# Kernel optimization log

Measured on AMD Instinct MI355X. Metric: run time of the kernel, lower is better.

## Reference

```python
import jax, jax.numpy as jnp
import numpy as np

N, EG, T, H, EC, L, NT = 10000, 200000, 300000, 128, 128, 3, 100


def _ssp(x):
    # ShiftedSoftplus: softplus(x) - log(2)
    return jax.nn.softplus(x) - jnp.log(2.0).astype(x.dtype)


def _bn(x, g, b):
    # BatchNorm1d in training mode: biased batch stats, eps=1e-5
    m = jnp.mean(x, axis=0)
    v = jnp.var(x, axis=0)
    return g * (x - m) * jax.lax.rsqrt(v + 1e-5) + b


def _forward(z, i, j, idx_i, idx_j, idx_k, idx_ji, idx_kj, pos,
             We1, be1, We2, be2, We3, be3,
             Wc1, bc1, g_c1, b_c1, g_n, b_n,
             Wc2, bc2, g_c2, b_c2, Wc3, bc3, g_c3, b_c3,
             g_c22, b_c22, g_c32, b_c32,
             Wf1, bf1, Wf2, bf2, Wf3, bf3):
    # AtomType2NodeEmb
    h = jax.nn.one_hot(z, NT, dtype=jnp.float32)
    h = _ssp(h @ We1 + be1)
    h = _ssp(h @ We2 + be2)
    node = h @ We3 + be3                      # [N, H]
    # geometry + GaussianFilter edge embedding
    rel = pos[i] - pos[j]                     # [EG, 3]
    dist = jnp.sqrt(jnp.sum(rel * rel, axis=-1))
    unit = rel / dist[:, None]
    offset = jnp.linspace(0.0, 5.0, EC)
    coeff = -0.5 / (offset[1] - offset[0]) ** 2
    edge = jnp.exp(coeff * (dist[:, None] - offset[None, :]) ** 2)  # [EG, EC]
    for l in range(L):
        # NodeUpdate
        c1 = jnp.concatenate([node[i], edge], axis=1) @ Wc1[l] + bc1[l]
        c1 = _bn(c1, g_c1[l], b_c1[l])
        f1, r1 = jnp.split(c1, 2, axis=1)
        agg = jax.ops.segment_sum(jax.nn.sigmoid(f1) * jnp.tanh(r1), i, num_segments=N)
        node = jnp.tanh(node + _bn(agg, g_n[l], b_n[l]))
        # EdgeUpdate: pair term
        c2 = (node[i] * node[j]) @ Wc2[l] + bc2[l]
        c2 = _bn(c2, g_c2[l], b_c2[l])
        f2, r2 = jnp.split(c2, 2, axis=1)
        c2_emb = _bn(jax.nn.sigmoid(f2) * jnp.tanh(r2), g_c22[l], b_c22[l])
        # EdgeUpdate: triplet term
        c3 = jnp.concatenate([node[idx_i], node[idx_j], node[idx_k],
                              edge[idx_ji], edge[idx_kj]], axis=1) @ Wc3[l] + bc3[l]
        c3 = _bn(c3, g_c3[l], b_c3[l])
        f3, r3 = jnp.split(c3, 2, axis=1)
        agg3 = jax.ops.segment_sum(jax.nn.sigmoid(f3) * jnp.tanh(r3), idx_ji, num_segments=EG)
        c3_emb = _bn(agg3, g_c32[l], b_c32[l])
        edge = jnp.tanh(edge + c2_emb + c3_emb)
    # ForcePredictor
    f = _ssp(edge @ Wf1 + bf1)
    f = _ssp(f @ Wf2 + bf2)
    force = (f @ Wf3 + bf3) * unit            # [EG, 3]
    return jax.ops.segment_sum(force, i, num_segments=N)


def setup_inputs() -> dict:
    ks = iter(jax.random.split(jax.random.key(0), 32))

    def w(shape):
        return jax.random.normal(next(ks), shape, jnp.float32) * (shape[-2] ** -0.5)

    z = jax.random.randint(next(ks), (N,), 0, NT)
    pos = jax.random.uniform(next(ks), (N, 3), jnp.float32) * 5.0
    i = jax.random.randint(next(ks), (EG,), 0, N)
    j = (i + 1 + jax.random.randint(next(ks), (EG,), 0, N - 1)) % N  # no self-loops
    idx_i = jax.random.randint(next(ks), (T,), 0, N)
    idx_j = jax.random.randint(next(ks), (T,), 0, N)
    idx_k = jax.random.randint(next(ks), (T,), 0, N)
    idx_ji = jax.random.randint(next(ks), (T,), 0, EG)
    idx_kj = jax.random.randint(next(ks), (T,), 0, EG)
    return dict(
        z=z, pos=pos, i=i, j=j, idx_i=idx_i, idx_j=idx_j, idx_k=idx_k,
        idx_ji=idx_ji, idx_kj=idx_kj,
        We1=w((NT, H)), be1=jnp.zeros((H,)), We2=w((H, H)), be2=jnp.zeros((H,)),
        We3=w((H, H)), be3=jnp.zeros((H,)),
        Wc1=w((L, H + EC, 2 * H)), bc1=jnp.zeros((L, 2 * H)),
        g_c1=jnp.ones((L, 2 * H)), b_c1=jnp.zeros((L, 2 * H)),
        g_n=jnp.ones((L, H)), b_n=jnp.zeros((L, H)),
        Wc2=w((L, H, 2 * EC)), bc2=jnp.zeros((L, 2 * EC)),
        g_c2=jnp.ones((L, 2 * EC)), b_c2=jnp.zeros((L, 2 * EC)),
        Wc3=w((L, 3 * H + 2 * EC, 2 * EC)), bc3=jnp.zeros((L, 2 * EC)),
        g_c3=jnp.ones((L, 2 * EC)), b_c3=jnp.zeros((L, 2 * EC)),
        g_c22=jnp.ones((L, EC)), b_c22=jnp.zeros((L, EC)),
        g_c32=jnp.ones((L, EC)), b_c32=jnp.zeros((L, EC)),
        Wf1=w((EC, EC)), bf1=jnp.zeros((EC,)), Wf2=w((EC, EC)), bf2=jnp.zeros((EC,)),
        Wf3=w((EC, 1)), bf3=jnp.zeros((1,)),
    )


def reference(z, pos, i, j, idx_i, idx_j, idx_k, idx_ji, idx_kj,
              We1, be1, We2, be2, We3, be3,
              Wc1, bc1, g_c1, b_c1, g_n, b_n,
              Wc2, bc2, g_c2, b_c2, Wc3, bc3, g_c3, b_c3,
              g_c22, b_c22, g_c32, b_c32,
              Wf1, bf1, Wf2, bf2, Wf3, bf3):
    return _forward(z, i, j, idx_i, idx_j, idx_k, idx_ji, idx_kj, pos,
                    We1, be1, We2, be2, We3, be3,
                    Wc1, bc1, g_c1, b_c1, g_n, b_n,
                    Wc2, bc2, g_c2, b_c2, Wc3, bc3, g_c3, b_c3,
                    g_c22, b_c22, g_c32, b_c32,
                    Wf1, bf1, Wf2, bf2, Wf3, bf3)
```

## Files before the change

kernel.cpp:

```cpp
#include <hip/hip_runtime.h>

typedef unsigned short u16;
typedef unsigned int   u32;
typedef __attribute__((ext_vector_type(8))) short short8;
typedef __attribute__((ext_vector_type(4))) float f32x4;

#define NN  10000
#define EGN 200000
#define TTN 300000
#define LLN 3

__device__ __forceinline__ float b2f(u16 u){ union{u32 i; float f;} x; x.i=(u32)u<<16; return x.f; }
__device__ __forceinline__ u16 f2b(float f){ union{float f; u32 u;} x; x.f=f; u32 r=(x.u + 0x7fffu + ((x.u>>16)&1u))>>16; return (u16)r; }
__device__ __forceinline__ float sigf(float x){ return 1.f/(1.f+__expf(-x)); }
__device__ __forceinline__ float tanhf_(float x){ float e=__expf(2.f*x); return 1.f - 2.f/(e+1.f); }
__device__ __forceinline__ float sspf(float x){ return fmaxf(x,0.f) + log1pf(__expf(-fabsf(x))) - 0.6931471805599453f; }

__device__ __forceinline__ void async16(void* lds, const void* g){
  __builtin_amdgcn_global_load_lds((const __attribute__((address_space(1))) void*)g,
                                   (__attribute__((address_space(3))) void*)lds, 16, 0, 0);
}
__device__ __forceinline__ void split_store(float v, u16* ph, u16* pl, size_t o){
  u16 h = f2b(v); ph[o] = h; pl[o] = f2b(v - b2f(h));
}
__device__ __forceinline__ short8 ldfrag(const u16* P, int row, int kk, int lane){
  int kg = kk*4 + (lane>>4);
  int slot = kg ^ (row&7);
  return *(const short8*)(P + row*64 + slot*8);
}

struct Segs {
  const u16* sh[10];
  const u16* sl[10];
  const int* idx[10];
  int coff[10];
};

template<int NP, int ROWS>
__device__ __forceinline__ void stageA(u16* Ah, u16* Al,
    const u16* sh, const u16* sl, const int* idxp, int coff,
    int rb, int M, int tid){
#pragma unroll
  for (int rnd=0; rnd<ROWS/32; ++rnd){
    int u = rnd*256 + tid;
    int row = u>>3, s = u&7, sw = s ^ (row&7);
    int grow = rb + row; if (grow >= M) grow = M-1;
    int srow = idxp ? idxp[grow] : grow;
    size_t go = (size_t)srow*256 + coff + sw*16;
    async16(Ah + u*8, (const char*)sh + go);
    if (NP==2) async16(Al + u*8, (const char*)sl + go);
  }
}

template<int NP, int ROWS>
__device__ __forceinline__ void stageA_prod(u16* Ah, u16* Al,
    const u16* nh, const u16* nl, const int* pii, const int* pjj,
    int rb, int M, int ks, int tid){
#pragma unroll
  for (int rep=0; rep<ROWS/64; ++rep){
    int row = rep*64 + (tid>>2), q = tid&3;
    int e = rb + row; if (e >= M) e = M-1;
    int ia = pii[e], ja = pjj[e];
    const u16* phi = nh + (size_t)ia*128 + ks*64 + q*16;
    const u16* pli = nl + (size_t)ia*128 + ks*64 + q*16;
    const u16* phj = nh + (size_t)ja*128 + ks*64 + q*16;
    const u16* plj = nl + (size_t)ja*128 + ks*64 + q*16;
#pragma unroll
    for (int c=0;c<2;c++){
      short8 hi = *(const short8*)(phi + c*8);
      short8 li = *(const short8*)(pli + c*8);
      short8 hj = *(const short8*)(phj + c*8);
      short8 lj = *(const short8*)(plj + c*8);
      short8 vh, vl;
#pragma unroll
      for (int k=0;k<8;k++){
        float a = b2f((u16)hi[k]) + b2f((u16)li[k]);
        float b = b2f((u16)hj[k]) + b2f((u16)lj[k]);
        float v = a*b;
        u16 h = f2b(v);
        vh[k] = (short)h;
        vl[k] = (short)f2b(v - b2f(h));
      }
      int g = q*2 + c, slot = g ^ (row&7);
      *(short8*)(Ah + row*64 + slot*8) = vh;
      if (NP==2) *(short8*)(Al + row*64 + slot*8) = vl;
    }
  }
}

template<int NP, int BROWS>
__device__ __forceinline__ void stageB_id(u16* Bh, u16* Bl,
    const u16* Wh, const u16* Wl, int K2b, int ksoff, int tid){
#pragma unroll
  for (int rnd=0; rnd<BROWS/32; ++rnd){
    int u = rnd*256 + tid;
    int row = u>>3, s = u&7, sw = s ^ (row&7);
    size_t go = (size_t)row*K2b + ksoff + sw*16;
    async16(Bh + u*8, (const char*)Wh + go);
    if (NP==2) async16(Bl + u*8, (const char*)Wl + go);
  }
}

template<int NP>
__device__ __forceinline__ void stageB_pair(u16* Bh, u16* Bl,
    const u16* Wh, const u16* Wl, int P0, int K2b, int ksoff, int tid){
#pragma unroll
  for (int rnd=0; rnd<4; ++rnd){
    int u = rnd*256 + tid;
    int row = u>>3, s = u&7, sw = s ^ (row&7);
    int wr = (row < 64) ? (P0 + row) : (128 + P0 + (row-64));
    size_t go = (size_t)wr*K2b + ksoff + sw*16;
    async16(Bh + u*8, (const char*)Wh + go);
    if (NP==2) async16(Bl + u*8, (const char*)Wl + go);
  }
}

template<bool PROD>
__global__ __launch_bounds__(256) void gemm_stats(
  int M, int nseg, Segs segs,
  const u16* __restrict__ nh, const u16* __restrict__ nl,
  const int* __restrict__ pii, const int* __restrict__ pjj,
  const u16* __restrict__ Wh, int K2b, const float* __restrict__ bias,
  float* __restrict__ st)
{
  __shared__ u16 Ah[64*64];
  __shared__ u16 Bh[256*64];
  __shared__ float ls[256], lq[256];
  const int tid = threadIdx.x, lane = tid&63, wv = tid>>6;
  const int rb = blockIdx.x*64;
  ls[tid]=0.f; lq[tid]=0.f;

  f32x4 acc[16];
#pragma unroll
  for (int n=0;n<16;n++) acc[n] = (f32x4){0.f,0.f,0.f,0.f};

  for (int ks=0; ks<nseg; ++ks){
    if (PROD) stageA_prod<1,64>(Ah, nullptr, nh, nl, pii, pjj, rb, M, ks, tid);
    else      stageA<1,64>(Ah, nullptr, segs.sh[ks], nullptr, segs.idx[ks], segs.coff[ks], rb, M, tid);
    stageB_id<1,256>(Bh, nullptr, Wh, nullptr, K2b, ks*128, tid);
    __syncthreads();
    const int arow = wv*16 + (lane&15);
#pragma unroll
    for (int kk=0;kk<2;kk++){
      short8 a = ldfrag(Ah, arow, kk, lane);
#pragma unroll
      for (int n=0;n<16;n++){
        short8 b = ldfrag(Bh, n*16 + (lane&15), kk, lane);
        acc[n] = __builtin_amdgcn_mfma_f32_16x16x32_bf16(a, b, acc[n], 0,0,0);
      }
    }
    __syncthreads();
  }
#pragma unroll
  for (int n=0;n<16;n++){
    float bb = bias[n*16 + (lane&15)];
    float s=0.f, q=0.f;
#pragma unroll
    for (int r=0;r<4;r++){
      int grow = rb + wv*16 + (lane>>4)*4 + r;
      if (grow < M){ float v = acc[n][r] + bb; s += v; q += v*v; }
    }
    s += __shfl_xor(s,16); s += __shfl_xor(s,32);
    q += __shfl_xor(q,16); q += __shfl_xor(q,32);
    if (lane < 16){ atomicAdd(&ls[n*16+lane], s); atomicAdd(&lq[n*16+lane], q); }
  }
  __syncthreads();
  atomicAdd(&st[tid], ls[tid]); atomicAdd(&st[256+tid], lq[tid]);
}

template<int NP, bool PROD, int EPI>
__global__ __launch_bounds__(256) void gemm_pair(
  int M, int nseg, Segs segs,
  const u16* __restrict__ nh, const u16* __restrict__ nl,
  const int* __restrict__ pii, const int* __restrict__ pjj,
  const u16* __restrict__ Wh, const u16* __restrict__ Wl, int K2b,
  const float* __restrict__ bias,
  const float* __restrict__ st, const float* __restrict__ g, const float* __restrict__ b, float inv,
  const int* __restrict__ sidx, float* __restrict__ aggout,
  const float* __restrict__ st22, const float* __restrict__ g22, const float* __restrict__ b22,
  const float* __restrict__ st32, const float* __restrict__ g32, const float* __restrict__ b32, float inv2,
  const float* __restrict__ agg3, u16* __restrict__ eh, u16* __restrict__ el,
  float* __restrict__ st22out)
{
  __shared__ u16 Ah[128*64];
  __shared__ u16 Al[NP==2 ? 128*64 : 64];
  __shared__ u16 Bh[128*64];
  __shared__ u16 Bl[NP==2 ? 128*64 : 64];
  __shared__ float ls[64], lq[64];
  __shared__ float sAf[64], sCf[64], sAr[64], sCr[64];
  __shared__ float sA22[64], sC22[64], sA32[64], sC32[64];
  const int tid = threadIdx.x, lane = tid&63, wv = tid>>6;
  const int wm = wv>>1, wn = wv&1;
  const int rb = blockIdx.x*128, P0 = blockIdx.y*64;

  if (tid < 64){
    int p = P0 + tid;
    float m1 = st[p]*inv,     v1 = st[256+p]*inv - m1*m1;
    float a1 = g[p]*rsqrtf(v1+1e-5f);
    sAf[tid]=a1; sCf[tid]=b[p]-a1*m1;
    float m2 = st[128+p]*inv, v2 = st[384+p]*inv - m2*m2;
    float a2 = g[128+p]*rsqrtf(v2+1e-5f);
    sAr[tid]=a2; sCr[tid]=b[128+p]-a2*m2;
    if (EPI==1){
      float m3 = st22[p]*inv2, v3 = st22[128+p]*inv2 - m3*m3;
      float a3 = g22[p]*rsqrtf(v3+1e-5f);
      sA22[tid]=a3; sC22[tid]=b22[p]-a3*m3;
      float m4 = st32[p]*inv2, v4 = st32[128+p]*inv2 - m4*m4;
      float a4 = g32[p]*rsqrtf(v4+1e-5f);
      sA32[tid]=a4; sC32[tid]=b32[p]-a4*m4;
    }
    if (EPI==2){ ls[tid]=0.f; lq[tid]=0.f; }
  }

  f32x4 accf[4][2], accr[4][2];
#pragma unroll
  for (int m=0;m<4;m++)
#pragma unroll
    for (int n=0;n<2;n++){ accf[m][n]=(f32x4){0.f,0.f,0.f,0.f}; accr[m][n]=(f32x4){0.f,0.f,0.f,0.f}; }

  for (int ks=0; ks<nseg; ++ks){
    if (PROD) stageA_prod<NP,128>(Ah, Al, nh, nl, pii, pjj, rb, M, ks, tid);
    else      stageA<NP,128>(Ah, Al, segs.sh[ks], segs.sl[ks], segs.idx[ks], segs.coff[ks], rb, M, tid);
    stageB_pair<NP>(Bh, Bl, Wh, Wl, P0, K2b, ks*128, tid);
    __syncthreads();
#pragma unroll
    for (int kk=0;kk<2;kk++){
      short8 ah[4], al[4];
#pragma unroll
      for (int m=0;m<4;m++){
        int ar = wm*64 + m*16 + (lane&15);
        ah[m] = ldfrag(Ah, ar, kk, lane);
        if constexpr (NP==2) al[m] = ldfrag(Al, ar, kk, lane);
      }
#pragma unroll
      for (int n=0;n<2;n++){
        int brf = wn*32 + n*16 + (lane&15);
        short8 bfh = ldfrag(Bh, brf,    kk, lane);
        short8 brh = ldfrag(Bh, 64+brf, kk, lane);
        short8 bfl, brl;
        if constexpr (NP==2){ bfl = ldfrag(Bl, brf, kk, lane); brl = ldfrag(Bl, 64+brf, kk, lane); }
#pragma unroll
        for (int m=0;m<4;m++){
          accf[m][n] = __builtin_amdgcn_mfma_f32_16x16x32_bf16(ah[m], bfh, accf[m][n], 0,0,0);
          accr[m][n] = __builtin_amdgcn_mfma_f32_16x16x32_bf16(ah[m], brh, accr[m][n], 0,0,0);
          if constexpr (NP==2){
            accf[m][n] = __builtin_amdgcn_mfma_f32_16x16x32_bf16(ah[m], bfl, accf[m][n], 0,0,0);
            accf[m][n] = __builtin_amdgcn_mfma_f32_16x16x32_bf16(al[m], bfh, accf[m][n], 0,0,0);
            accr[m][n] = __builtin_amdgcn_mfma_f32_16x16x32_bf16(ah[m], brl, accr[m][n], 0,0,0);
            accr[m][n] = __builtin_amdgcn_mfma_f32_16x16x32_bf16(al[m], brh, accr[m][n], 0,0,0);
          }
        }
      }
    }
    __syncthreads();
  }

#pragma unroll
  for (int n=0;n<2;n++){
    const int pp = wn*32 + n*16 + (lane&15);
    const int p  = P0 + pp;
    const float bf_ = bias[p], br_ = bias[128+p];
    const float Af = sAf[pp], Cf = sCf[pp], Ar = sAr[pp], Cr = sCr[pp];
    float su=0.f, sq=0.f;
#pragma unroll
    for (int m=0;m<4;m++){
#pragma unroll
      for (int r=0;r<4;r++){
        int grow = rb + wm*64 + m*16 + (lane>>4)*4 + r;
        if (grow < M){
          float yf = accf[m][n][r] + bf_;
          float yr = accr[m][n][r] + br_;
          float u = sigf(Af*yf + Cf) * tanhf_(Ar*yr + Cr);
          if (EPI==0){
            atomicAdd(&aggout[(size_t)sidx[grow]*128 + p], u);
          } else if (EPI==1){
            size_t o = (size_t)grow*128 + p;
            float eo = b2f(eh[o]) + b2f(el[o]);
            float v = tanhf_(eo + sA22[pp]*u + sC22[pp] + sA32[pp]*agg3[o] + sC32[pp]);
            split_store(v, eh, el, o);
          } else {
            su += u; sq += u*u;
          }
        }
      }
    }
    if (EPI==2){
      su += __shfl_xor(su,16); su += __shfl_xor(su,32);
      sq += __shfl_xor(sq,16); sq += __shfl_xor(sq,32);
      if (lane < 16){ atomicAdd(&ls[wn*32+n*16+lane], su); atomicAdd(&lq[wn*32+n*16+lane], sq); }
    }
  }
  if (EPI==2){
    __syncthreads();
    if (tid < 64){ atomicAdd(&st22out[P0+tid], ls[tid]); atomicAdd(&st22out[128+P0+tid], lq[tid]); }
  }
}

__global__ __launch_bounds__(256) void gemm_force(
  int M, Segs segs,
  const u16* __restrict__ Wh, const u16* __restrict__ Wl, int K2b,
  const float* __restrict__ bias, u16* __restrict__ oh, u16* __restrict__ ol)
{
  __shared__ u16 Ah[64*64], Al[64*64];
  __shared__ u16 Bh[128*64], Bl[128*64];
  const int tid = threadIdx.x, lane = tid&63, wv = tid>>6;
  const int rb = blockIdx.x*64;

  f32x4 acc[8];
#pragma unroll
  for (int n=0;n<8;n++) acc[n] = (f32x4){0.f,0.f,0.f,0.f};

  for (int ks=0; ks<2; ++ks){
    stageA<2,64>(Ah, Al, segs.sh[ks], segs.sl[ks], segs.idx[ks], segs.coff[ks], rb, M, tid);
    stageB_id<2,128>(Bh, Bl, Wh, Wl, K2b, ks*128, tid);
    __syncthreads();
    const int arow = wv*16 + (lane&15);
#pragma unroll
    for (int kk=0;kk<2;kk++){
      short8 ah = ldfrag(Ah, arow, kk, lane);
      short8 al = ldfrag(Al, arow, kk, lane);
#pragma unroll
      for (int n=0;n<8;n++){
        int br = n*16 + (lane&15);
        short8 bh = ldfrag(Bh, br, kk, lane);
        short8 bl = ldfrag(Bl, br, kk, lane);
        acc[n] = __builtin_amdgcn_mfma_f32_16x16x32_bf16(ah, bh, acc[n], 0,0,0);
        acc[n] = __builtin_amdgcn_mfma_f32_16x16x32_bf16(ah, bl, acc[n], 0,0,0);
        acc[n] = __builtin_amdgcn_mfma_f32_16x16x32_bf16(al, bh, acc[n], 0,0,0);
      }
    }
    __syncthreads();
  }
#pragma unroll
  for (int n=0;n<8;n++){
    int col = n*16 + (lane&15);
    float bb = bias[col];
#pragma unroll
    for (int r=0;r<4;r++){
      int grow = rb + wv*16 + (lane>>4)*4 + r;
      if (grow < M){
        float v = sspf(acc[n][r] + bb);
        split_store(v, oh, ol, (size_t)grow*128 + col);
      }
    }
  }
}

__global__ void transpose_cvt(const float* __restrict__ src, u16* __restrict__ dh, u16* __restrict__ dl, int K, int N){
  __shared__ float t[32][33];
  const float* s = src + (size_t)blockIdx.z * K * N;
  u16* dsth = dh + (size_t)blockIdx.z * K * N;
  u16* dstl = dl + (size_t)blockIdx.z * K * N;
  int n0 = blockIdx.x*32, k0 = blockIdx.y*32;
  for (int dy=threadIdx.y; dy<32; dy+=8){
    int k = k0+dy, n = n0+threadIdx.x;
    if (k<K && n<N) t[dy][threadIdx.x] = s[(size_t)k*N + n];
  }
  __syncthreads();
  for (int dy=threadIdx.y; dy<32; dy+=8){
    int n = n0+dy, k = k0+threadIdx.x;
    if (n<N && k<K) split_store(t[threadIdx.x][dy], dsth, dstl, (size_t)n*K + k);
  }
}

__global__ __launch_bounds__(128) void embed_k(const int* __restrict__ z,
  const float* __restrict__ We1, const float* __restrict__ be1,
  const float* __restrict__ We2, const float* __restrict__ be2,
  const float* __restrict__ We3, const float* __restrict__ be3,
  u16* __restrict__ nh, u16* __restrict__ nl){
  __shared__ float h0[128], h1[128];
  int nid = blockIdx.x, t = threadIdx.x;
  int zz = z[nid];
  h0[t] = sspf(We1[zz*128 + t] + be1[t]);
  __syncthreads();
  float a = be2[t];
  for (int k=0;k<128;k++) a += h0[k]*We2[k*128+t];
  h1[t] = sspf(a);
  __syncthreads();
  float b = be3[t];
  for (int k=0;k<128;k++) b += h1[k]*We3[k*128+t];
  split_store(b, nh, nl, (size_t)nid*128+t);
}

__global__ __launch_bounds__(256) void geom_k(const float* __restrict__ pos,
  const int* __restrict__ ii, const int* __restrict__ jj,
  float* __restrict__ unitv, u16* __restrict__ eh, u16* __restrict__ el){
  int t = threadIdx.x; int e = blockIdx.x*2 + (t>>7); int col = t&127;
  int a = ii[e], b = jj[e];
  float dx = pos[a*3]-pos[b*3], dy=pos[a*3+1]-pos[b*3+1], dz=pos[a*3+2]-pos[b*3+2];
  float dist = sqrtf(dx*dx+dy*dy+dz*dz);
  if (col==0){ float inv=1.f/dist; unitv[e*3]=dx*inv; unitv[e*3+1]=dy*inv; unitv[e*3+2]=dz*inv; }
  const float step = 5.0f/127.0f;
  const float coeff = -0.5f/(step*step);
  float d = dist - step*(float)col;
  float g = __expf(coeff*d*d);
  split_store(g, eh, el, (size_t)e*128+col);
}

__global__ __launch_bounds__(256) void colstats128(const float* __restrict__ m, int M, float* __restrict__ st){
  __shared__ float ls[128], lq[128];
  int t=threadIdx.x; if(t<128){ls[t]=0.f;lq[t]=0.f;} __syncthreads();
  int col=t&127, hf=t>>7; float ps=0.f,pq=0.f;
  int npair=(M+1)>>1;
  for (int pr=blockIdx.x; pr<npair; pr+=gridDim.x){
    int row=pr*2+hf;
    if(row<M){ float v=m[(size_t)row*128+col]; ps+=v; pq+=v*v; }
  }
  atomicAdd(&ls[col],ps); atomicAdd(&lq[col],pq);
  __syncthreads();
  if(t<128){ atomicAdd(&st[t],ls[t]); atomicAdd(&st[128+t],lq[t]); }
}

__global__ __launch_bounds__(256) void node_update_k(u16* __restrict__ nh, u16* __restrict__ nl,
  const float* __restrict__ agg, const float* __restrict__ st,
  const float* __restrict__ g, const float* __restrict__ b, float inv, int Nn)
{
  int t=threadIdx.x; int col=t&127, hf=t>>7;
  float mean = st[col]*inv;
  float var  = st[128+col]*inv - mean*mean;
  float A = g[col]*rsqrtf(var+1e-5f);
  float C = b[col] - A*mean;
  int npair=(Nn+1)>>1;
  for (int pr=blockIdx.x; pr<npair; pr+=gridDim.x){
    int row=pr*2+hf; if(row>=Nn) continue;
    size_t o=(size_t)row*128+col;
    float nv = b2f(nh[o]) + b2f(nl[o]);
    float v = tanhf_(nv + A*agg[o] + C);
    split_store(v, nh, nl, o);
  }
}

__global__ __launch_bounds__(256) void force_k(const u16* __restrict__ fh, const u16* __restrict__ fl,
  const float* __restrict__ Wf3, const float* __restrict__ bf3,
  const float* __restrict__ unitv, const int* __restrict__ ii, float* __restrict__ outp, int Me)
{
  int wv=threadIdx.x>>6, lane=threadIdx.x&63;
  int e = blockIdx.x*4 + wv; if(e>=Me) return;
  size_t o0=(size_t)e*128+lane, o1=o0+64;
  float p = (b2f(fh[o0])+b2f(fl[o0]))*Wf3[lane] + (b2f(fh[o1])+b2f(fl[o1]))*Wf3[64+lane];
  for (int s=32;s>0;s>>=1) p += __shfl_down(p, s);
  if (lane==0){
    float F = p + bf3[0];
    atomicAdd(&outp[ii[e]*3+0], F*unitv[e*3+0]);
    atomicAdd(&outp[ii[e]*3+1], F*unitv[e*3+1]);
    atomicAdd(&outp[ii[e]*3+2], F*unitv[e*3+2]);
  }
}

__global__ void sentinel_k(float* o, int n, float v){
  int i = blockIdx.x*256 + threadIdx.x; if (i<n) o[i]=v;
}

extern "C" void kernel_launch(void* const* d_in, const int* in_sizes, int n_in,
                              void* d_out, int out_size, void* d_ws, size_t ws_size,
                              hipStream_t stream)
{
  (void)in_sizes; (void)n_in;
  const int* z      = (const int*)d_in[0];
  const float* pos  = (const float*)d_in[1];
  const int* ii     = (const int*)d_in[2];
  const int* jj     = (const int*)d_in[3];
  const int* idx_i  = (const int*)d_in[4];
  const int* idx_j  = (const int*)d_in[5];
  const int* idx_k  = (const int*)d_in[6];
  const int* idx_ji = (const int*)d_in[7];
  const int* idx_kj = (const int*)d_in[8];
  const float* We1=(const float*)d_in[9];  const float* be1=(const float*)d_in[10];
  const float* We2=(const float*)d_in[11]; const float* be2=(const float*)d_in[12];
  const float* We3=(const float*)d_in[13]; const float* be3=(const float*)d_in[14];
  const float* Wc1=(const float*)d_in[15]; const float* bc1=(const float*)d_in[16];
  const float* g_c1=(const float*)d_in[17]; const float* b_c1=(const float*)d_in[18];
  const float* g_n=(const float*)d_in[19]; const float* b_n=(const float*)d_in[20];
  const float* Wc2=(const float*)d_in[21]; const float* bc2=(const float*)d_in[22];
  const float* g_c2=(const float*)d_in[23]; const float* b_c2=(const float*)d_in[24];
  const float* Wc3=(const float*)d_in[25]; const float* bc3=(const float*)d_in[26];
  const float* g_c3=(const float*)d_in[27]; const float* b_c3=(const float*)d_in[28];
  const float* g_c22=(const float*)d_in[29]; const float* b_c22=(const float*)d_in[30];
  const float* g_c32=(const float*)d_in[31]; const float* b_c32=(const float*)d_in[32];
  const float* Wf1=(const float*)d_in[33]; const float* bf1=(const float*)d_in[34];
  const float* Wf2=(const float*)d_in[35]; const float* bf2=(const float*)d_in[36];
  const float* Wf3=(const float*)d_in[37]; const float* bf3=(const float*)d_in[38];

  char* ws = (char*)d_ws;
  size_t off=0;
  auto alloc=[&](size_t b){ size_t o=off; off += (b+255)&~(size_t)255; return o; };
  u16*   node_h = (u16*)(ws + alloc((size_t)NN*128*2));
  u16*   node_l = (u16*)(ws + alloc((size_t)NN*128*2));
  u16*   edge_h = (u16*)(ws + alloc((size_t)EGN*128*2));
  u16*   edge_l = (u16*)(ws + alloc((size_t)EGN*128*2));
  float* unitv  = (float*)(ws + alloc((size_t)EGN*3*4));
  float* agg    = (float*)(ws + alloc((size_t)NN*128*4));
  float* agg3   = (float*)(ws + alloc((size_t)EGN*128*4));
  u16*   wc1h   = (u16*)(ws + alloc((size_t)3*256*256*2));
  u16*   wc1l   = (u16*)(ws + alloc((size_t)3*256*256*2));
  u16*   wc2h   = (u16*)(ws + alloc((size_t)3*256*128*2));
  u16*   wc2l   = (u16*)(ws + alloc((size_t)3*256*128*2));
  u16*   wc3h   = (u16*)(ws + alloc((size_t)3*256*640*2));
  u16*   wc3l   = (u16*)(ws + alloc((size_t)3*256*640*2));
  u16*   wf1h   = (u16*)(ws + alloc((size_t)128*128*2));
  u16*   wf1l   = (u16*)(ws + alloc((size_t)128*128*2));
  u16*   wf2h   = (u16*)(ws + alloc((size_t)128*128*2));
  u16*   wf2l   = (u16*)(ws + alloc((size_t)128*128*2));
  float* stats  = (float*)(ws + alloc(2304*4));

  if (off > ws_size){
    sentinel_k<<<(out_size+255)/256, 256, 0, stream>>>((float*)d_out, out_size, 123456.0f);
    return;
  }

  float* st1 = stats;
  float* st2 = stats+512;
  float* st3 = stats+1024;
  float* stN = stats+1536;
  float* st32= stats+1792;
  float* st22= stats+2048;

  u16* f1h = (u16*)agg3;
  u16* f1l = f1h + (size_t)EGN*128;
  u16* f2h = edge_h;
  u16* f2l = edge_l;

  hipMemsetAsync(d_out, 0, (size_t)out_size*4, stream);

  dim3 tb(32,8);
  transpose_cvt<<<dim3(8,8,3),  tb, 0, stream>>>(Wc1, wc1h, wc1l, 256, 256);
  transpose_cvt<<<dim3(8,4,3),  tb, 0, stream>>>(Wc2, wc2h, wc2l, 128, 256);
  transpose_cvt<<<dim3(8,20,3), tb, 0, stream>>>(Wc3, wc3h, wc3l, 640, 256);
  transpose_cvt<<<dim3(4,4,1),  tb, 0, stream>>>(Wf1, wf1h, wf1l, 128, 128);
  transpose_cvt<<<dim3(4,4,1),  tb, 0, stream>>>(Wf2, wf2h, wf2l, 128, 128);

  embed_k<<<NN,128,0,stream>>>(z, We1,be1,We2,be2,We3,be3, node_h, node_l);
  geom_k<<<EGN/2,256,0,stream>>>(pos, ii, jj, unitv, edge_h, edge_l);

  const int gE64  = (EGN+63)/64;
  const int gT64  = (TTN+63)/64;
  const int gE128 = (EGN+127)/128;
  const int gT128 = (TTN+127)/128;
  Segs dummy{};
  const float invE = 1.0f/EGN, invT = 1.0f/TTN, invN = 1.0f/NN;

  for (int l=0;l<LLN;l++){
    hipMemsetAsync(stats, 0, 2304*4, stream);
    hipMemsetAsync(agg,  0, (size_t)NN*128*4, stream);
    hipMemsetAsync(agg3, 0, (size_t)EGN*128*4, stream);

    const u16* w1h = wc1h + l*256*256; const u16* w1l = wc1l + l*256*256;
    const u16* w2h = wc2h + l*256*128; const u16* w2l = wc2l + l*256*128;
    const u16* w3h = wc3h + l*256*640; const u16* w3l = wc3l + l*256*640;

    Segs s1{};
    s1.sh[0]=node_h; s1.sl[0]=node_l; s1.idx[0]=ii;      s1.coff[0]=0;
    s1.sh[1]=node_h; s1.sl[1]=node_l; s1.idx[1]=ii;      s1.coff[1]=128;
    s1.sh[2]=edge_h; s1.sl[2]=edge_l; s1.idx[2]=nullptr; s1.coff[2]=0;
    s1.sh[3]=edge_h; s1.sl[3]=edge_l; s1.idx[3]=nullptr; s1.coff[3]=128;
    gemm_stats<false><<<gE64,256,0,stream>>>(EGN, 4, s1, nullptr,nullptr,nullptr,nullptr,
                                             w1h, 512, bc1+l*256, st1);
    gemm_pair<2,false,0><<<dim3(gE128,2),256,0,stream>>>(EGN, 4, s1, nullptr,nullptr,nullptr,nullptr,
        w1h, w1l, 512, bc1+l*256,
        st1, g_c1+l*256, b_c1+l*256, invE,
        ii, agg,
        nullptr,nullptr,nullptr, nullptr,nullptr,nullptr, 0.f,
        nullptr, nullptr, nullptr, nullptr);
    colstats128<<<256,256,0,stream>>>(agg, NN, stN);
    node_update_k<<<2048,256,0,stream>>>(node_h, node_l, agg, stN, g_n+l*128, b_n+l*128, invN, NN);

    Segs s3{};
    s3.sh[0]=node_h; s3.sl[0]=node_l; s3.idx[0]=idx_i;  s3.coff[0]=0;
    s3.sh[1]=node_h; s3.sl[1]=node_l; s3.idx[1]=idx_i;  s3.coff[1]=128;
    s3.sh[2]=node_h; s3.sl[2]=node_l; s3.idx[2]=idx_j;  s3.coff[2]=0;
    s3.sh[3]=node_h; s3.sl[3]=node_l; s3.idx[3]=idx_j;  s3.coff[3]=128;
    s3.sh[4]=node_h; s3.sl[4]=node_l; s3.idx[4]=idx_k;  s3.coff[4]=0;
    s3.sh[5]=node_h; s3.sl[5]=node_l; s3.idx[5]=idx_k;  s3.coff[5]=128;
    s3.sh[6]=edge_h; s3.sl[6]=edge_l; s3.idx[6]=idx_ji; s3.coff[6]=0;
    s3.sh[7]=edge_h; s3.sl[7]=edge_l; s3.idx[7]=idx_ji; s3.coff[7]=128;
    s3.sh[8]=edge_h; s3.sl[8]=edge_l; s3.idx[8]=idx_kj; s3.coff[8]=0;
    s3.sh[9]=edge_h; s3.sl[9]=edge_l; s3.idx[9]=idx_kj; s3.coff[9]=128;
    gemm_stats<false><<<gT64,256,0,stream>>>(TTN, 10, s3, nullptr,nullptr,nullptr,nullptr,
                                             w3h, 1280, bc3+l*256, st3);
    gemm_pair<2,false,0><<<dim3(gT128,2),256,0,stream>>>(TTN, 10, s3, nullptr,nullptr,nullptr,nullptr,
        w3h, w3l, 1280, bc3+l*256,
        st3, g_c3+l*256, b_c3+l*256, invT,
        idx_ji, agg3,
        nullptr,nullptr,nullptr, nullptr,nullptr,nullptr, 0.f,
        nullptr, nullptr, nullptr, nullptr);
    colstats128<<<1024,256,0,stream>>>(agg3, EGN, st32);

    gemm_stats<true><<<gE64,256,0,stream>>>(EGN, 2, dummy, node_h,node_l,ii,jj,
                                            w2h, 256, bc2+l*256, st2);
    gemm_pair<1,true,2><<<dim3(gE128,2),256,0,stream>>>(EGN, 2, dummy, node_h,node_l,ii,jj,
        w2h, nullptr, 256, bc2+l*256,
        st2, g_c2+l*256, b_c2+l*256, invE,
        nullptr, nullptr,
        nullptr,nullptr,nullptr, nullptr,nullptr,nullptr, 0.f,
        nullptr, nullptr, nullptr, st22);
    gemm_pair<2,true,1><<<dim3(gE128,2),256,0,stream>>>(EGN, 2, dummy, node_h,node_l,ii,jj,
        w2h, w2l, 256, bc2+l*256,
        st2, g_c2+l*256, b_c2+l*256, invE,
        nullptr, nullptr,
        st22, g_c22+l*128, b_c22+l*128, st32, g_c32+l*128, b_c32+l*128, invE,
        agg3, edge_h, edge_l, nullptr);
  }

  Segs sf1{}; sf1.sh[0]=edge_h; sf1.sl[0]=edge_l; sf1.idx[0]=nullptr; sf1.coff[0]=0;
              sf1.sh[1]=edge_h; sf1.sl[1]=edge_l; sf1.idx[1]=nullptr; sf1.coff[1]=128;
  gemm_force<<<gE64,256,0,stream>>>(EGN, sf1, wf1h, wf1l, 256, bf1, f1h, f1l);
  Segs sf2{}; sf2.sh[0]=f1h; sf2.sl[0]=f1l; sf2.idx[0]=nullptr; sf2.coff[0]=0;
              sf2.sh[1]=f1h; sf2.sl[1]=f1l; sf2.idx[1]=nullptr; sf2.coff[1]=128;
  gemm_force<<<gE64,256,0,stream>>>(EGN, sf2, wf2h, wf2l, 256, bf2, f2h, f2l);
  force_k<<<(EGN+3)/4,256,0,stream>>>(f2h, f2l, Wf3, bf3, unitv, ii, (float*)d_out, EGN);
}
```

Before: 4.618 ms.

## Precompute per-node weight projections instead of GEMMing gathered node rows

The node part of each concat-matmul, which is linear in gathered node rows, is now computed once per node with small GEMMs into fp32 projection tables. The edge and triplet GEMMs then handle only the edge segments, which cuts the K dimension from 512 to 256 for c1 and from 1280 to 512 for c3. The node contribution is added back in the epilogues by gathering rows from the fp32 tables. This trades a large amount of MFMA work and gathered bf16 A-staging for scattered fp32 gathers in the epilogue and extra workspace.

After: 6.870 ms. +48.8%, slower.

```diff
diff --git a/kernel.cpp b/kernel.cpp
--- a/kernel.cpp
+++ b/kernel.cpp
@@ -30,10 +30,15 @@
 }
 
 struct Segs {
-  const u16* sh[10];
-  const u16* sl[10];
-  const int* idx[10];
-  int coff[10];
+  const u16* sh[4];
+  const u16* sl[4];
+  const int* idx[4];
+  int coff[4];
+};
+struct PNG {
+  const float* p0; const float* p1; const float* p2;
+  const int* g0; const int* g1; const int* g2;
+  int n;
 };
 
 template<int NP, int ROWS>
@@ -121,7 +126,7 @@
   const u16* __restrict__ nh, const u16* __restrict__ nl,
   const int* __restrict__ pii, const int* __restrict__ pjj,
   const u16* __restrict__ Wh, int K2b, const float* __restrict__ bias,
-  float* __restrict__ st)
+  float* __restrict__ st, PNG png)
 {
   __shared__ u16 Ah[64*64];
   __shared__ u16 Bh[256*64];
@@ -151,14 +156,32 @@
     }
     __syncthreads();
   }
+
+  int growr[4]; int s0[4], s1[4], s2[4];
+#pragma unroll
+  for (int r=0;r<4;r++){
+    int gr = rb + wv*16 + (lane>>4)*4 + r; growr[r]=gr;
+    s0[r]=s1[r]=s2[r]=0;
+    if (gr < M){
+      if (png.n>0) s0[r]=png.g0[gr];
+      if (png.n>1) s1[r]=png.g1[gr];
+      if (png.n>2) s2[r]=png.g2[gr];
+    }
+  }
 #pragma unroll
   for (int n=0;n<16;n++){
-    float bb = bias[n*16 + (lane&15)];
+    int col = n*16 + (lane&15);
+    float bb = bias[col];
     float s=0.f, q=0.f;
 #pragma unroll
     for (int r=0;r<4;r++){
-      int grow = rb + wv*16 + (lane>>4)*4 + r;
-      if (grow < M){ float v = acc[n][r] + bb; s += v; q += v*v; }
+      if (growr[r] < M){
+        float v = acc[n][r] + bb;
+        if (png.n>0) v += png.p0[(size_t)s0[r]*256 + col];
+        if (png.n>1) v += png.p1[(size_t)s1[r]*256 + col];
+        if (png.n>2) v += png.p2[(size_t)s2[r]*256 + col];
+        s += v; q += v*v;
+      }
     }
     s += __shfl_xor(s,16); s += __shfl_xor(s,32);
     q += __shfl_xor(q,16); q += __shfl_xor(q,32);
@@ -180,7 +203,7 @@
   const float* __restrict__ st22, const float* __restrict__ g22, const float* __restrict__ b22,
   const float* __restrict__ st32, const float* __restrict__ g32, const float* __restrict__ b32, float inv2,
   const float* __restrict__ agg3, u16* __restrict__ eh, u16* __restrict__ el,
-  float* __restrict__ st22out)
+  float* __restrict__ st22out, PNG png)
 {
   __shared__ u16 Ah[128*64];
   __shared__ u16 Al[NP==2 ? 128*64 : 64];
@@ -255,56 +278,67 @@
     __syncthreads();
   }
 
-#pragma unroll
-  for (int n=0;n<2;n++){
-    const int pp = wn*32 + n*16 + (lane&15);
-    const int p  = P0 + pp;
-    const float bf_ = bias[p], br_ = bias[128+p];
-    const float Af = sAf[pp], Cf = sCf[pp], Ar = sAr[pp], Cr = sCr[pp];
-    float su=0.f, sq=0.f;
-#pragma unroll
-    for (int m=0;m<4;m++){
-#pragma unroll
-      for (int r=0;r<4;r++){
-        int grow = rb + wm*64 + m*16 + (lane>>4)*4 + r;
-        if (grow < M){
-          float yf = accf[m][n][r] + bf_;
-          float yr = accr[m][n][r] + br_;
-          float u = sigf(Af*yf + Cf) * tanhf_(Ar*yr + Cr);
-          if (EPI==0){
-            atomicAdd(&aggout[(size_t)sidx[grow]*128 + p], u);
-          } else if (EPI==1){
-            size_t o = (size_t)grow*128 + p;
-            float eo = b2f(eh[o]) + b2f(el[o]);
-            float v = tanhf_(eo + sA22[pp]*u + sC22[pp] + sA32[pp]*agg3[o] + sC32[pp]);
-            split_store(v, eh, el, o);
-          } else {
-            su += u; sq += u*u;
-          }
+  float su[2]={0.f,0.f}, sq[2]={0.f,0.f};
+#pragma unroll
+  for (int m=0;m<4;m++){
+#pragma unroll
+    for (int r=0;r<4;r++){
+      int grow = rb + wm*64 + m*16 + (lane>>4)*4 + r;
+      if (grow >= M) continue;
+      int c0=0,c1=0,c2=0,sv=0;
+      if (png.n>0) c0 = png.g0[grow];
+      if (png.n>1) c1 = png.g1[grow];
+      if (png.n>2) c2 = png.g2[grow];
+      if (EPI==0) sv = sidx[grow];
+#pragma unroll
+      for (int n=0;n<2;n++){
+        const int pp = wn*32 + n*16 + (lane&15);
+        const int p  = P0 + pp;
+        float yf = accf[m][n][r] + bias[p];
+        float yr = accr[m][n][r] + bias[128+p];
+        if (png.n>0){ yf += png.p0[(size_t)c0*256 + p]; yr += png.p0[(size_t)c0*256 + 128 + p]; }
+        if (png.n>1){ yf += png.p1[(size_t)c1*256 + p]; yr += png.p1[(size_t)c1*256 + 128 + p]; }
+        if (png.n>2){ yf += png.p2[(size_t)c2*256 + p]; yr += png.p2[(size_t)c2*256 + 128 + p]; }
+        float u = sigf(sAf[pp]*yf + sCf[pp]) * tanhf_(sAr[pp]*yr + sCr[pp]);
+        if (EPI==0){
+          atomicAdd(&aggout[(size_t)sv*128 + p], u);
+        } else if (EPI==1){
+          size_t o = (size_t)grow*128 + p;
+          float eo = b2f(eh[o]) + b2f(el[o]);
+          float v = tanhf_(eo + sA22[pp]*u + sC22[pp] + sA32[pp]*agg3[o] + sC32[pp]);
+          split_store(v, eh, el, o);
+        } else {
+          su[n] += u; sq[n] += u*u;
         }
       }
     }
-    if (EPI==2){
-      su += __shfl_xor(su,16); su += __shfl_xor(su,32);
-      sq += __shfl_xor(sq,16); sq += __shfl_xor(sq,32);
-      if (lane < 16){ atomicAdd(&ls[wn*32+n*16+lane], su); atomicAdd(&lq[wn*32+n*16+lane], sq); }
-    }
   }
   if (EPI==2){
+#pragma unroll
+    for (int n=0;n<2;n++){
+      float s = su[n], q = sq[n];
+      s += __shfl_xor(s,16); s += __shfl_xor(s,32);
+      q += __shfl_xor(q,16); q += __shfl_xor(q,32);
+      if (lane < 16){ atomicAdd(&ls[wn*32+n*16+lane], s); atomicAdd(&lq[wn*32+n*16+lane], q); }
+    }
     __syncthreads();
     if (tid < 64){ atomicAdd(&st22out[P0+tid], ls[tid]); atomicAdd(&st22out[128+P0+tid], lq[tid]); }
   }
 }
 
+template<int FOUT>
 __global__ __launch_bounds__(256) void gemm_force(
   int M, Segs segs,
   const u16* __restrict__ Wh, const u16* __restrict__ Wl, int K2b,
-  const float* __restrict__ bias, u16* __restrict__ oh, u16* __restrict__ ol)
+  const float* __restrict__ bias, u16* __restrict__ oh, u16* __restrict__ ol,
+  float* __restrict__ of, int ostr)
 {
   __shared__ u16 Ah[64*64], Al[64*64];
   __shared__ u16 Bh[128*64], Bl[128*64];
   const int tid = threadIdx.x, lane = tid&63, wv = tid>>6;
-  const int rb = blockIdx.x*64;
+  const int rb = blockIdx.x*64, cb = blockIdx.y*128;
+  const u16* Whb = Wh + (size_t)cb*(K2b>>1);
+  const u16* Wlb = Wl + (size_t)cb*(K2b>>1);
 
   f32x4 acc[8];
 #pragma unroll
@@ -312,7 +346,7 @@
 
   for (int ks=0; ks<2; ++ks){
     stageA<2,64>(Ah, Al, segs.sh[ks], segs.sl[ks], segs.idx[ks], segs.coff[ks], rb, M, tid);
-    stageB_id<2,128>(Bh, Bl, Wh, Wl, K2b, ks*128, tid);
+    stageB_id<2,128>(Bh, Bl, Whb, Wlb, K2b, ks*128, tid);
     __syncthreads();
     const int arow = wv*16 + (lane&15);
 #pragma unroll
@@ -334,32 +368,37 @@
 #pragma unroll
   for (int n=0;n<8;n++){
     int col = n*16 + (lane&15);
-    float bb = bias[col];
+    float bb = (FOUT==0) ? bias[col] : 0.f;
 #pragma unroll
     for (int r=0;r<4;r++){
       int grow = rb + wv*16 + (lane>>4)*4 + r;
       if (grow < M){
-        float v = sspf(acc[n][r] + bb);
-        split_store(v, oh, ol, (size_t)grow*128 + col);
-      }
-    }
-  }
-}
-
-__global__ void transpose_cvt(const float* __restrict__ src, u16* __restrict__ dh, u16* __restrict__ dl, int K, int N){
+        if (FOUT==0){
+          float v = sspf(acc[n][r] + bb);
+          split_store(v, oh, ol, (size_t)grow*128 + col);
+        } else {
+          of[(size_t)grow*ostr + cb + col] = acc[n][r];
+        }
+      }
+    }
+  }
+}
+
+__global__ void transpose_cvt(const float* __restrict__ src, u16* __restrict__ dh, u16* __restrict__ dl,
+                              int K, int N, int rowOff, int sLS, int dKS, int dKOff, int dLS){
   __shared__ float t[32][33];
-  const float* s = src + (size_t)blockIdx.z * K * N;
-  u16* dsth = dh + (size_t)blockIdx.z * K * N;
-  u16* dstl = dl + (size_t)blockIdx.z * K * N;
+  src += (size_t)blockIdx.z * sLS;
+  u16* dsth = dh + (size_t)blockIdx.z * dLS;
+  u16* dstl = dl + (size_t)blockIdx.z * dLS;
   int n0 = blockIdx.x*32, k0 = blockIdx.y*32;
   for (int dy=threadIdx.y; dy<32; dy+=8){
     int k = k0+dy, n = n0+threadIdx.x;
-    if (k<K && n<N) t[dy][threadIdx.x] = s[(size_t)k*N + n];
+    if (k<K && n<N) t[dy][threadIdx.x] = src[(size_t)(rowOff+k)*N + n];
   }
   __syncthreads();
   for (int dy=threadIdx.y; dy<32; dy+=8){
     int n = n0+dy, k = k0+threadIdx.x;
-    if (n<N && k<K) split_store(t[threadIdx.x][dy], dsth, dstl, (size_t)n*K + k);
+    if (n<N && k<K) split_store(t[threadIdx.x][dy], dsth, dstl, (size_t)n*dKS + dKOff + k);
   }
 }
 
@@ -483,7 +522,7 @@
 
   char* ws = (char*)d_ws;
   size_t off=0;
-  auto alloc=[&](size_t b){ size_t o=off; off += (b+255)&~(size_t)255; return o; };
+  auto alloc=[&](size_t bb){ size_t o=off; off += (bb+255)&~(size_t)255; return o; };
   u16*   node_h = (u16*)(ws + alloc((size_t)NN*128*2));
   u16*   node_l = (u16*)(ws + alloc((size_t)NN*128*2));
   u16*   edge_h = (u16*)(ws + alloc((size_t)EGN*128*2));
@@ -491,12 +530,18 @@
   float* unitv  = (float*)(ws + alloc((size_t)EGN*3*4));
   float* agg    = (float*)(ws + alloc((size_t)NN*128*4));
   float* agg3   = (float*)(ws + alloc((size_t)EGN*128*4));
-  u16*   wc1h   = (u16*)(ws + alloc((size_t)3*256*256*2));
-  u16*   wc1l   = (u16*)(ws + alloc((size_t)3*256*256*2));
+  float* PN1    = (float*)(ws + alloc((size_t)NN*256*4));
+  float* PN3    = (float*)(ws + alloc((size_t)3*NN*256*4));
+  u16*   wc1eh  = (u16*)(ws + alloc((size_t)3*256*128*2));
+  u16*   wc1el  = (u16*)(ws + alloc((size_t)3*256*128*2));
+  u16*   wc1nh  = (u16*)(ws + alloc((size_t)3*256*128*2));
+  u16*   wc1nl  = (u16*)(ws + alloc((size_t)3*256*128*2));
   u16*   wc2h   = (u16*)(ws + alloc((size_t)3*256*128*2));
   u16*   wc2l   = (u16*)(ws + alloc((size_t)3*256*128*2));
-  u16*   wc3h   = (u16*)(ws + alloc((size_t)3*256*640*2));
-  u16*   wc3l   = (u16*)(ws + alloc((size_t)3*256*640*2));
+  u16*   wc3nh  = (u16*)(ws + alloc((size_t)3*3*256*128*2));
+  u16*   wc3nl  = (u16*)(ws + alloc((size_t)3*3*256*128*2));
+  u16*   wc3eh  = (u16*)(ws + alloc((size_t)3*256*256*2));
+  u16*   wc3el  = (u16*)(ws + alloc((size_t)3*256*256*2));
   u16*   wf1h   = (u16*)(ws + alloc((size_t)128*128*2));
   u16*   wf1l   = (u16*)(ws + alloc((size_t)128*128*2));
   u16*   wf2h   = (u16*)(ws + alloc((size_t)128*128*2));
@@ -523,11 +568,15 @@
   hipMemsetAsync(d_out, 0, (size_t)out_size*4, stream);
 
   dim3 tb(32,8);
-  transpose_cvt<<<dim3(8,8,3),  tb, 0, stream>>>(Wc1, wc1h, wc1l, 256, 256);
-  transpose_cvt<<<dim3(8,4,3),  tb, 0, stream>>>(Wc2, wc2h, wc2l, 128, 256);
-  transpose_cvt<<<dim3(8,20,3), tb, 0, stream>>>(Wc3, wc3h, wc3l, 640, 256);
-  transpose_cvt<<<dim3(4,4,1),  tb, 0, stream>>>(Wf1, wf1h, wf1l, 128, 128);
-  transpose_cvt<<<dim3(4,4,1),  tb, 0, stream>>>(Wf2, wf2h, wf2l, 128, 128);
+  transpose_cvt<<<dim3(8,4,3), tb, 0, stream>>>(Wc1, wc1eh, wc1el, 128,256, 128, 65536, 128, 0, 32768);
+  transpose_cvt<<<dim3(8,4,3), tb, 0, stream>>>(Wc1, wc1nh, wc1nl, 128,256, 0,   65536, 128, 0, 32768);
+  transpose_cvt<<<dim3(8,4,3), tb, 0, stream>>>(Wc2, wc2h,  wc2l,  128,256, 0,   32768, 128, 0, 32768);
+  for (int t=0;t<3;t++)
+    transpose_cvt<<<dim3(8,4,3), tb, 0, stream>>>(Wc3, wc3nh + t*32768, wc3nl + t*32768, 128,256, t*128, 163840, 128, 0, 98304);
+  transpose_cvt<<<dim3(8,4,3), tb, 0, stream>>>(Wc3, wc3eh, wc3el, 128,256, 384, 163840, 256, 0,   65536);
+  transpose_cvt<<<dim3(8,4,3), tb, 0, stream>>>(Wc3, wc3eh, wc3el, 128,256, 512, 163840, 256, 128, 65536);
+  transpose_cvt<<<dim3(4,4,1), tb, 0, stream>>>(Wf1, wf1h, wf1l, 128,128, 0, 16384, 128, 0, 16384);
+  transpose_cvt<<<dim3(4,4,1), tb, 0, stream>>>(Wf2, wf2h, wf2l, 128,128, 0, 16384, 128, 0, 16384);
 
   embed_k<<<NN,128,0,stream>>>(z, We1,be1,We2,be2,We3,be3, node_h, node_l);
   geom_k<<<EGN/2,256,0,stream>>>(pos, ii, jj, unitv, edge_h, edge_l);
@@ -536,76 +585,80 @@
   const int gT64  = (TTN+63)/64;
   const int gE128 = (EGN+127)/128;
   const int gT128 = (TTN+127)/128;
+  const int gN64  = (NN+63)/64;
   Segs dummy{};
+  PNG  png0{};
   const float invE = 1.0f/EGN, invT = 1.0f/TTN, invN = 1.0f/NN;
+
+  Segs segNode{};
+  segNode.sh[0]=node_h; segNode.sl[0]=node_l; segNode.idx[0]=nullptr; segNode.coff[0]=0;
+  segNode.sh[1]=node_h; segNode.sl[1]=node_l; segNode.idx[1]=nullptr; segNode.coff[1]=128;
+
+  Segs segEdge{};
+  segEdge.sh[0]=edge_h; segEdge.sl[0]=edge_l; segEdge.idx[0]=nullptr; segEdge.coff[0]=0;
+  segEdge.sh[1]=edge_h; segEdge.sl[1]=edge_l; segEdge.idx[1]=nullptr; segEdge.coff[1]=128;
+
+  Segs segE3{};
+  segE3.sh[0]=edge_h; segE3.sl[0]=edge_l; segE3.idx[0]=idx_ji; segE3.coff[0]=0;
+  segE3.sh[1]=edge_h; segE3.sl[1]=edge_l; segE3.idx[1]=idx_ji; segE3.coff[1]=128;
+  segE3.sh[2]=edge_h; segE3.sl[2]=edge_l; segE3.idx[2]=idx_kj; segE3.coff[2]=0;
+  segE3.sh[3]=edge_h; segE3.sl[3]=edge_l; segE3.idx[3]=idx_kj; segE3.coff[3]=128;
 
   for (int l=0;l<LLN;l++){
     hipMemsetAsync(stats, 0, 2304*4, stream);
     hipMemsetAsync(agg,  0, (size_t)NN*128*4, stream);
     hipMemsetAsync(agg3, 0, (size_t)EGN*128*4, stream);
 
-    const u16* w1h = wc1h + l*256*256; const u16* w1l = wc1l + l*256*256;
-    const u16* w2h = wc2h + l*256*128; const u16* w2l = wc2l + l*256*128;
-    const u16* w3h = wc3h + l*256*640; const u16* w3l = wc3l + l*256*640;
-
-    Segs s1{};
-    s1.sh[0]=node_h; s1.sl[0]=node_l; s1.idx[0]=ii;      s1.coff[0]=0;
-    s1.sh[1]=node_h; s1.sl[1]=node_l; s1.idx[1]=ii;      s1.coff[1]=128;
-    s1.sh[2]=edge_h; s1.sl[2]=edge_l; s1.idx[2]=nullptr; s1.coff[2]=0;
-    s1.sh[3]=edge_h; s1.sl[3]=edge_l; s1.idx[3]=nullptr; s1.coff[3]=128;
-    gemm_stats<false><<<gE64,256,0,stream>>>(EGN, 4, s1, nullptr,nullptr,nullptr,nullptr,
-                                             w1h, 512, bc1+l*256, st1);
-    gemm_pair<2,false,0><<<dim3(gE128,2),256,0,stream>>>(EGN, 4, s1, nullptr,nullptr,nullptr,nullptr,
-        w1h, w1l, 512, bc1+l*256,
+    gemm_force<1><<<dim3(gN64,2),256,0,stream>>>(NN, segNode, wc1nh + l*32768, wc1nl + l*32768, 256,
+                                                 nullptr, nullptr, nullptr, PN1, 256);
+    PNG png1{PN1,nullptr,nullptr, ii,nullptr,nullptr, 1};
+    gemm_stats<false><<<gE64,256,0,stream>>>(EGN, 2, segEdge, nullptr,nullptr,nullptr,nullptr,
+                                             wc1eh + l*32768, 256, bc1+l*256, st1, png1);
+    gemm_pair<2,false,0><<<dim3(gE128,2),256,0,stream>>>(EGN, 2, segEdge, nullptr,nullptr,nullptr,nullptr,
+        wc1eh + l*32768, wc1el + l*32768, 256, bc1+l*256,
         st1, g_c1+l*256, b_c1+l*256, invE,
         ii, agg,
         nullptr,nullptr,nullptr, nullptr,nullptr,nullptr, 0.f,
-        nullptr, nullptr, nullptr, nullptr);
+        nullptr, nullptr, nullptr, nullptr, png1);
     colstats128<<<256,256,0,stream>>>(agg, NN, stN);
     node_update_k<<<2048,256,0,stream>>>(node_h, node_l, agg, stN, g_n+l*128, b_n+l*128, invN, NN);
 
-    Segs s3{};
-    s3.sh[0]=node_h; s3.sl[0]=node_l; s3.idx[0]=idx_i;  s3.coff[0]=0;
-    s3.sh[1]=node_h; s3.sl[1]=node_l; s3.idx[1]=idx_i;  s3.coff[1]=128;
-    s3.sh[2]=node_h; s3.sl[2]=node_l; s3.idx[2]=idx_j;  s3.coff[2]=0;
-    s3.sh[3]=node_h; s3.sl[3]=node_l; s3.idx[3]=idx_j;  s3.coff[3]=128;
-    s3.sh[4]=node_h; s3.sl[4]=node_l; s3.idx[4]=idx_k;  s3.coff[4]=0;
-    s3.sh[5]=node_h; s3.sl[5]=node_l; s3.idx[5]=idx_k;  s3.coff[5]=128;
-    s3.sh[6]=edge_h; s3.sl[6]=edge_l; s3.idx[6]=idx_ji; s3.coff[6]=0;
-    s3.sh[7]=edge_h; s3.sl[7]=edge_l; s3.idx[7]=idx_ji; s3.coff[7]=128;
-    s3.sh[8]=edge_h; s3.sl[8]=edge_l; s3.idx[8]=idx_kj; s3.coff[8]=0;
-    s3.sh[9]=edge_h; s3.sl[9]=edge_l; s3.idx[9]=idx_kj; s3.coff[9]=128;
-    gemm_stats<false><<<gT64,256,0,stream>>>(TTN, 10, s3, nullptr,nullptr,nullptr,nullptr,
-                                             w3h, 1280, bc3+l*256, st3);
-    gemm_pair<2,false,0><<<dim3(gT128,2),256,0,stream>>>(TTN, 10, s3, nullptr,nullptr,nullptr,nullptr,
-        w3h, w3l, 1280, bc3+l*256,
+    for (int t=0;t<3;t++)
+      gemm_force<1><<<dim3(gN64,2),256,0,stream>>>(NN, segNode,
+          wc3nh + l*98304 + t*32768, wc3nl + l*98304 + t*32768, 256,
+          nullptr, nullptr, nullptr, PN3 + (size_t)t*NN*256, 256);
+    PNG png3{PN3, PN3 + (size_t)NN*256, PN3 + (size_t)2*NN*256, idx_i, idx_j, idx_k, 3};
+    gemm_stats<false><<<gT64,256,0,stream>>>(TTN, 4, segE3, nullptr,nullptr,nullptr,nullptr,
+                                             wc3eh + l*65536, 512, bc3+l*256, st3, png3);
+    gemm_pair<2,false,0><<<dim3(gT128,2),256,0,stream>>>(TTN, 4, segE3, nullptr,nullptr,nullptr,nullptr,
+        wc3eh + l*65536, wc3el + l*65536, 512, bc3+l*256,
         st3, g_c3+l*256, b_c3+l*256, invT,
         idx_ji, agg3,
         nullptr,nullptr,nullptr, nullptr,nullptr,nullptr, 0.f,
-        nullptr, nullptr, nullptr, nullptr);
+        nullptr, nullptr, nullptr, nullptr, png3);
     colstats128<<<1024,256,0,stream>>>(agg3, EGN, st32);
 
     gemm_stats<true><<<gE64,256,0,stream>>>(EGN, 2, dummy, node_h,node_l,ii,jj,
-                                            w2h, 256, bc2+l*256, st2);
+                                            wc2h + l*32768, 256, bc2+l*256, st2, png0);
     gemm_pair<1,true,2><<<dim3(gE128,2),256,0,stream>>>(EGN, 2, dummy, node_h,node_l,ii,jj,
-        w2h, nullptr, 256, bc2+l*256,
+        wc2h + l*32768, nullptr, 256, bc2+l*256,
         st2, g_c2+l*256, b_c2+l*256, invE,
         nullptr, nullptr,
         nullptr,nullptr,nullptr, nullptr,nullptr,nullptr, 0.f,
-        nullptr, nullptr, nullptr, st22);
+        nullptr, nullptr, nullptr, st22, png0);
     gemm_pair<2,true,1><<<dim3(gE128,2),256,0,stream>>>(EGN, 2, dummy, node_h,node_l,ii,jj,
-        w2h, w2l, 256, bc2+l*256,
+        wc2h + l*32768, wc2l + l*32768, 256, bc2+l*256,
         st2, g_c2+l*256, b_c2+l*256, invE,
         nullptr, nullptr,
         st22, g_c22+l*128, b_c22+l*128, st32, g_c32+l*128, b_c32+l*128, invE,
-        agg3, edge_h, edge_l, nullptr);
+        agg3, edge_h, edge_l, nullptr, png0);
   }
 
   Segs sf1{}; sf1.sh[0]=edge_h; sf1.sl[0]=edge_l; sf1.idx[0]=nullptr; sf1.coff[0]=0;
               sf1.sh[1]=edge_h; sf1.sl[1]=edge_l; sf1.idx[1]=nullptr; sf1.coff[1]=128;
-  gemm_force<<<gE64,256,0,stream>>>(EGN, sf1, wf1h, wf1l, 256, bf1, f1h, f1l);
+  gemm_force<0><<<dim3(gE64,1),256,0,stream>>>(EGN, sf1, wf1h, wf1l, 256, bf1, f1h, f1l, nullptr, 0);
   Segs sf2{}; sf2.sh[0]=f1h; sf2.sl[0]=f1l; sf2.idx[0]=nullptr; sf2.coff[0]=0;
               sf2.sh[1]=f1h; sf2.sl[1]=f1l; sf2.idx[1]=nullptr; sf2.coff[1]=128;
-  gemm_force<<<gE64,256,0,stream>>>(EGN, sf2, wf2h, wf2l, 256, bf2, f2h, f2l);
+  gemm_force<0><<<dim3(gE64,1),256,0,stream>>>(EGN, sf2, wf2h, wf2l, 256, bf2, f2h, f2l, nullptr, 0);
   force_k<<<(EGN+3)/4,256,0,stream>>>(f2h, f2l, Wf3, bf3, unitv, ii, (float*)d_out, EGN);
 }
```
